# Optimization experiments

Hardware: AMD Instinct MI355X
Metric: run time of the kernel (lower is better)

## Reference

```python
import jax, jax.numpy as jnp
import numpy as np

B, T, D = 16, 4096, 256
CODEBOOK_SIZE = 1024
COMMITMENT = 1.0


def setup_inputs() -> dict:
    key = jax.random.key(0)
    kx, kc = jax.random.split(key)
    x = jax.random.normal(kx, (B, T, D), dtype=jnp.float32)
    codebook = jax.random.normal(kc, (CODEBOOK_SIZE, D), dtype=jnp.float32)
    return {"x": x, "codebook": codebook}


def reference(x, codebook):
    # x: [B, T, D] continuous latents; codebook: [K, D]
    flat = x.reshape(-1, x.shape[-1])  # [N, D]
    # does not affect argmin but is kept for faithfulness to torch.cdist-style math)
    x_sq = jnp.sum(flat * flat, axis=1, keepdims=True)            # [N, 1]
    c_sq = jnp.sum(codebook * codebook, axis=1)                   # [K]
    dist = x_sq - 2.0 * (flat @ codebook.T) + c_sq[None, :]       # [N, K]
    indices = jnp.argmin(dist, axis=1)                            # [N] int
    quantized = codebook[indices].reshape(x.shape)                # gather, [B, T, D]
    # commitment loss: encoder pulled toward (stopped) codes
    commit_loss = COMMITMENT * jnp.mean(
        (x - jax.lax.stop_gradient(quantized)) ** 2
    )
    # straight-through estimator
    out = x + jax.lax.stop_gradient(quantized - x)
    return out, indices.reshape(x.shape[:-1]), commit_loss
```

## Files before the change

### kernel.cpp

```cpp
#include <hip/hip_runtime.h>

#define N_TOK 65536
#define DIM   256
#define KCODE 1024

#define NTHREADS 256
#define TM 128
#define TN 128
#define BK 32
#define NCHUNK 8
#define NSTAGE 8
#define OTM 128

#define REFINE_EPS 0.125f
#define TIE_THETA 1.0e-4

#define WS_CSQ_OFF   16
#define WS_IDX_OFF   2048
#define WS_PAIRS_OFF (WS_IDX_OFF + N_TOK)
#define WS_CBPK_OFF  (WS_PAIRS_OFF + N_TOK * NCHUNK * 4)

typedef float f32x4  __attribute__((ext_vector_type(4)));
typedef short bf16x8 __attribute__((ext_vector_type(8)));
typedef short s16x8  __attribute__((ext_vector_type(8)));

__global__ void rowsq_np_kernel(const float* __restrict__ m,
                                float* __restrict__ out,
                                float* __restrict__ loss_ws, int rows) {
#pragma clang fp contract(off)
    if (blockIdx.x == 0 && threadIdx.x == 0) loss_ws[0] = 0.0f;
    int row = blockIdx.x * 16 + (threadIdx.x >> 4);
    int l   = threadIdx.x & 15;
    if (row >= rows) return;
    int h = l >> 3;
    int j = l & 7;
    const float* p = m + (size_t)row * DIM + h * 128 + j;
    float v = p[0];
    float r = v * v;
#pragma unroll
    for (int i = 1; i < 16; ++i) {
        float w  = p[i * 8];
        float w2 = w * w;
        r = r + w2;
    }
    float t = r + __shfl_xor(r, 1);
    t = t + __shfl_xor(t, 2);
    t = t + __shfl_xor(t, 4);
    t = t + __shfl_xor(t, 8);
    if (l == 0) out[row] = t;
}

__device__ __forceinline__ void ins2(float d, int idx,
                                     float& d1, int& i1, float& d2, int& i2) {
    if (d < d1 || (d == d1 && idx < i1)) {
        d2 = d1; i2 = i1; d1 = d; i1 = idx;
    } else if ((d < d2 || (d == d2 && idx < i2)) && idx != i1) {
        d2 = d; i2 = idx;
    }
}

__device__ __forceinline__ void f2bf_split(float v, short& hi, short& lo) {
    unsigned u = __float_as_uint(v);
    unsigned r = (u + 0x7fffu + ((u >> 16) & 1u)) >> 16;
    hi = (short)r;
    float hf = __uint_as_float(r << 16);
    float lf = v - hf;
    unsigned u2 = __float_as_uint(lf);
    unsigned r2 = (u2 + 0x7fffu + ((u2 >> 16) & 1u)) >> 16;
    lo = (short)r2;
}

__global__ void pack_tiles_kernel(const float* __restrict__ src,
                                  unsigned short* __restrict__ dst,
                                  int total) {
    int tid = blockIdx.x * blockDim.x + threadIdx.x;
    if (tid >= total) return;
    int s   = tid & 3;
    int r   = (tid >> 2) & 127;
    int kc  = (tid >> 9) & 7;
    int g   = tid >> 12;
    int oct = s ^ ((r >> 1) & 3);

    const float4* xr = reinterpret_cast<const float4*>(
        src + ((size_t)(g * 128 + r)) * DIM + kc * 32 + oct * 8);
    float4 v0 = xr[0];
    float4 v1 = xr[1];

    float f[8] = {v0.x, v0.y, v0.z, v0.w, v1.x, v1.y, v1.z, v1.w};
    s16x8 hv, lv;
#pragma unroll
    for (int i = 0; i < 8; ++i) {
        short h, l;
        f2bf_split(f[i], h, l);
        hv[i] = h; lv[i] = l;
    }
    size_t base_hi = (((size_t)(g * 16 + kc) * 128 + r) << 5) + s * 8;
    size_t base_lo = (((size_t)(g * 16 + 8 + kc) * 128 + r) << 5) + s * 8;
    *reinterpret_cast<s16x8*>(dst + base_hi) = hv;
    *reinterpret_cast<s16x8*>(dst + base_lo) = lv;
}

__device__ __forceinline__ void gload_lds16(const unsigned short* g, unsigned short* lds) {
    __builtin_amdgcn_global_load_lds(
        (const __attribute__((address_space(1))) unsigned int*)g,
        (__attribute__((address_space(3))) unsigned int*)lds, 16, 0, 0);
}

__launch_bounds__(NTHREADS, 2)
__global__ void vq_main_kernel(const unsigned short* __restrict__ xpk,
                               const unsigned short* __restrict__ cbpk,
                               const float* __restrict__ csq,
                               float4* __restrict__ pairs) {
    __shared__ __align__(16) unsigned short shbuf[2][4 * 4096];
    __shared__ float4 pairs_sh[TM][2];

    const int tid  = threadIdx.x;
    const int w    = tid >> 6;
    const int wy   = w >> 1;
    const int wx   = w & 1;
    const int lane = tid & 63;
    const int lm   = lane & 15;
    const int q    = lane >> 4;

    const int bx     = blockIdx.x;
    const int jj     = bx >> 3;
    const int grp    = (bx & 7) + ((jj >> 3) << 3);
    const int cchunk = jj & 7;
    const int tok0   = grp * TM;
    const int code0  = cchunk * TN;

    float cs_reg[4];
#pragma unroll
    for (int ni = 0; ni < 4; ++ni)
        cs_reg[ni] = csq[code0 + wx * 64 + ni * 16 + lm];

    f32x4 acc[4][4];
#pragma unroll
    for (int mi = 0; mi < 4; ++mi)
#pragma unroll
        for (int ni = 0; ni < 4; ++ni)
            acc[mi][ni] = (f32x4){0.f, 0.f, 0.f, 0.f};

    int offA[4], offB[4];
#pragma unroll
    for (int mi = 0; mi < 4; ++mi) {
        int r = wy * 64 + mi * 16 + lm;
        offA[mi] = r * BK + ((q ^ ((r >> 1) & 3)) * 8);
    }
#pragma unroll
    for (int ni = 0; ni < 4; ++ni) {
        int r = wx * 64 + ni * 16 + lm;
        offB[ni] = r * BK + ((q ^ ((r >> 1) & 3)) * 8);
    }

    const int lsrc = w * 1024 + lane * 8;
    auto stage = [&](int p, int kc) {
        const unsigned short* gah = xpk  + (((size_t)(grp    * 16 +     kc)) << 12) + lsrc;
        const unsigned short* gal = xpk  + (((size_t)(grp    * 16 + 8 + kc)) << 12) + lsrc;
        const unsigned short* gbh = cbpk + (((size_t)(cchunk * 16 +     kc)) << 12) + lsrc;
        const unsigned short* gbl = cbpk + (((size_t)(cchunk * 16 + 8 + kc)) << 12) + lsrc;
        unsigned short* base = &shbuf[p][w * 1024];
        gload_lds16(gah,       base);
        gload_lds16(gah + 512, base + 512);
        gload_lds16(gal,       base + 4096);
        gload_lds16(gal + 512, base + 4096 + 512);
        gload_lds16(gbh,       base + 8192);
        gload_lds16(gbh + 512, base + 8192 + 512);
        gload_lds16(gbl,       base + 12288);
        gload_lds16(gbl + 512, base + 12288 + 512);
    };

    stage(0, 0);
    __syncthreads();

    int p = 0;
#pragma unroll 1
    for (int kc = 0; kc < NSTAGE; ++kc) {
        if (kc < NSTAGE - 1) stage(p ^ 1, kc + 1);

        const unsigned short* buf = &shbuf[p][0];
        bf16x8 ah[4], al[4], bh[4], bl[4];
#pragma unroll
        for (int mi = 0; mi < 4; ++mi) {
            ah[mi] = *reinterpret_cast<const bf16x8*>(buf + offA[mi]);
            al[mi] = *reinterpret_cast<const bf16x8*>(buf + 4096 + offA[mi]);
        }
#pragma unroll
        for (int ni = 0; ni < 4; ++ni) {
            bh[ni] = *reinterpret_cast<const bf16x8*>(buf + 8192 + offB[ni]);
            bl[ni] = *reinterpret_cast<const bf16x8*>(buf + 12288 + offB[ni]);
        }

        __builtin_amdgcn_s_setprio(1);
#pragma unroll
        for (int mi = 0; mi < 4; ++mi)
#pragma unroll
            for (int ni = 0; ni < 4; ++ni)
                acc[mi][ni] = __builtin_amdgcn_mfma_f32_16x16x32_bf16(
                    ah[mi], bh[ni], acc[mi][ni], 0, 0, 0);
#pragma unroll
        for (int mi = 0; mi < 4; ++mi)
#pragma unroll
            for (int ni = 0; ni < 4; ++ni)
                acc[mi][ni] = __builtin_amdgcn_mfma_f32_16x16x32_bf16(
                    ah[mi], bl[ni], acc[mi][ni], 0, 0, 0);
#pragma unroll
        for (int mi = 0; mi < 4; ++mi)
#pragma unroll
            for (int ni = 0; ni < 4; ++ni)
                acc[mi][ni] = __builtin_amdgcn_mfma_f32_16x16x32_bf16(
                    al[mi], bh[ni], acc[mi][ni], 0, 0, 0);
        __builtin_amdgcn_s_setprio(0);

        __syncthreads();
        p ^= 1;
    }

#pragma unroll
    for (int mi = 0; mi < 4; ++mi) {
#pragma unroll
        for (int r = 0; r < 4; ++r) {
            int row_local = wy * 64 + mi * 16 + q * 4 + r;
            float l1 = 3.4e38f, l2 = 3.4e38f;
            int   j1 = 0x7fffffff, j2 = 0x7fffffff;
#pragma unroll
            for (int ni = 0; ni < 4; ++ni) {
                float d = cs_reg[ni] - 2.0f * acc[mi][ni][r];
                ins2(d, code0 + wx * 64 + ni * 16 + lm, l1, j1, l2, j2);
            }
#pragma unroll
            for (int m = 1; m < 16; m <<= 1) {
                float o1 = __shfl_xor(l1, m);
                int   p1 = __shfl_xor(j1, m);
                float o2 = __shfl_xor(l2, m);
                int   p2 = __shfl_xor(j2, m);
                ins2(o1, p1, l1, j1, l2, j2);
                ins2(o2, p2, l1, j1, l2, j2);
            }
            if (lm == 0) {
                float4 pr;
                pr.x = l1; pr.y = l2;
                pr.z = __int_as_float(j1); pr.w = __int_as_float(j2);
                pairs_sh[row_local][wx] = pr;
            }
        }
    }
    __syncthreads();
    if (tid < TM) {
        float4 pa = pairs_sh[tid][0];
        float4 pb = pairs_sh[tid][1];
        float d1 = pa.x, d2 = pa.y;
        int   i1 = __float_as_int(pa.z), i2 = __float_as_int(pa.w);
        ins2(pb.x, __float_as_int(pb.z), d1, i1, d2, i2);
        ins2(pb.y, __float_as_int(pb.w), d1, i1, d2, i2);
        float4 pr;
        pr.x = d1; pr.y = d2;
        pr.z = __int_as_float(i1); pr.w = __int_as_float(i2);
        pairs[(size_t)cchunk * N_TOK + tok0 + tid] = pr;
    }
}

__launch_bounds__(256)
__global__ void merge_output_kernel(const float* __restrict__ x,
                                    const float* __restrict__ cb,
                                    const float4* __restrict__ pairs,
                                    float* __restrict__ out_q,
                                    float* __restrict__ out_idx,
                                    float* __restrict__ loss_ws) {
    __shared__ int   sh_idx[OTM];
    __shared__ float wsum[4];
    const int tid  = threadIdx.x;
    const int tok0 = blockIdx.x * OTM;

    if (tid < OTM) {
        const int t = tok0 + tid;
        float4 p0 = pairs[t];
        float d1 = p0.x, d2 = p0.y;
        int   i1 = __float_as_int(p0.z), i2 = __float_as_int(p0.w);
#pragma unroll
        for (int c = 1; c < NCHUNK; ++c) {
            float4 p = pairs[(size_t)c * N_TOK + t];
            ins2(p.x, __float_as_int(p.z), d1, i1, d2, i2);
            ins2(p.y, __float_as_int(p.w), d1, i1, d2, i2);
        }

        int pick = i1;
        if (d2 - d1 < REFINE_EPS) {
            const float* xr = x + (size_t)t * DIM;
            const float* c1 = cb + (size_t)i1 * DIM;
            const float* c2 = cb + (size_t)i2 * DIM;
            double sA = 0.0, dA = 0.0, sB = 0.0, dB = 0.0;
            for (int k = 0; k < DIM; ++k) {
                double xv = (double)xr[k];
                double a  = (double)c1[k];
                double b  = (double)c2[k];
                sA += a * a; dA += xv * a;
                sB += b * b; dB += xv * b;
            }
            double DA  = sA - 2.0 * dA;
            double DB  = sB - 2.0 * dB;
            double gap = DB - DA;
            if (gap > TIE_THETA)       pick = i1;
            else if (gap < -TIE_THETA) pick = i2;
            else                       pick = (i1 < i2) ? i1 : i2;
        }
        sh_idx[tid] = pick;
        out_idx[t]  = (float)pick;
    }
    __syncthreads();

    float lsum = 0.0f;
    for (int t = 0; t < OTM; ++t) {
        int code = sh_idx[t];
        float qv = cb[(size_t)code * DIM + tid];
        float xv = x[(size_t)(tok0 + t) * DIM + tid];
        out_q[(size_t)(tok0 + t) * DIM + tid] = xv + (qv - xv);
        float df = xv - qv;
        lsum = fmaf(df, df, lsum);
    }

#pragma unroll
    for (int off = 1; off < 64; off <<= 1) lsum += __shfl_xor(lsum, off);
    if ((tid & 63) == 0) wsum[tid >> 6] = lsum;
    __syncthreads();
    if (tid == 0) atomicAdd(loss_ws, (wsum[0] + wsum[1]) + (wsum[2] + wsum[3]));
}

__global__ void finalize_kernel(const float* ws, float* out_loss) {
    if (threadIdx.x == 0) out_loss[0] = ws[0] * (1.0f / 16777216.0f);
}

extern "C" void kernel_launch(void* const* d_in, const int* in_sizes, int n_in,
                              void* d_out, int out_size, void* d_ws, size_t ws_size,
                              hipStream_t stream) {
    const float* x  = (const float*)d_in[0];
    const float* cb = (const float*)d_in[1];

    float* out      = (float*)d_out;
    float* out_q    = out;
    float* out_idx  = out + (size_t)N_TOK * DIM;
    float* out_loss = out_idx + N_TOK;

    float*  ws    = (float*)d_ws;
    float*  csq   = ws + WS_CSQ_OFF;
    float4* pairs = (float4*)(ws + WS_PAIRS_OFF);
    unsigned short* cbpk = (unsigned short*)(ws + WS_CBPK_OFF);
    unsigned short* xpk  = (unsigned short*)out_q;

    rowsq_np_kernel<<<KCODE / 16, 256, 0, stream>>>(cb, csq, ws, KCODE);
    pack_tiles_kernel<<<(N_TOK * 32) / 256, 256, 0, stream>>>(x, xpk, N_TOK * 32);
    pack_tiles_kernel<<<(KCODE * 32) / 256, 256, 0, stream>>>(cb, cbpk, KCODE * 32);
    vq_main_kernel<<<(N_TOK / TM) * NCHUNK, NTHREADS, 0, stream>>>(xpk, cbpk, csq, pairs);
    merge_output_kernel<<<N_TOK / OTM, 256, 0, stream>>>(x, cb, pairs, out_q, out_idx, ws);
    finalize_kernel<<<1, 64, 0, stream>>>(ws, out_loss);
}
```

Baseline: 889.1 us.

## Stream codebook operands from global/L2 and stage only token tiles in LDS

The main GEMM kernel no longer stages codebook tiles in LDS. Each wave reads its codebook fragments directly from global memory, which is expected to hit L2 because the codebook is small. Only token tiles are double-buffered in shared memory, with the codebook pack left unswizzled to match. The three bf16 split-precision products (hi*hi, hi*lo, lo*hi) are serialized into 24 stages of 16 MFMAs each, which shrinks LDS and register footprint so launch bounds can target 4 blocks per CU. The trade-off is more barriers per block and global-load latency on the B operand inside the loop.

```diff
diff --git a/kernel.cpp b/kernel.cpp
--- a/kernel.cpp
+++ b/kernel.cpp
@@ -9,7 +9,7 @@
 #define TN 128
 #define BK 32
 #define NCHUNK 8
-#define NSTAGE 8
+#define NSTAGE 24
 #define OTM 128
 
 #define REFINE_EPS 0.125f
@@ -72,14 +72,14 @@
 
 __global__ void pack_tiles_kernel(const float* __restrict__ src,
                                   unsigned short* __restrict__ dst,
-                                  int total) {
+                                  int total, int swz) {
     int tid = blockIdx.x * blockDim.x + threadIdx.x;
     if (tid >= total) return;
     int s   = tid & 3;
     int r   = (tid >> 2) & 127;
     int kc  = (tid >> 9) & 7;
     int g   = tid >> 12;
-    int oct = s ^ ((r >> 1) & 3);
+    int oct = swz ? (s ^ ((r >> 1) & 3)) : s;
 
     const float4* xr = reinterpret_cast<const float4*>(
         src + ((size_t)(g * 128 + r)) * DIM + kc * 32 + oct * 8);
@@ -106,12 +106,12 @@
         (__attribute__((address_space(3))) unsigned int*)lds, 16, 0, 0);
 }
 
-__launch_bounds__(NTHREADS, 2)
+__launch_bounds__(NTHREADS, 4)
 __global__ void vq_main_kernel(const unsigned short* __restrict__ xpk,
                                const unsigned short* __restrict__ cbpk,
                                const float* __restrict__ csq,
                                float4* __restrict__ pairs) {
-    __shared__ __align__(16) unsigned short shbuf[2][4 * 4096];
+    __shared__ __align__(16) unsigned short shbuf[2][TM * BK];
     __shared__ float4 pairs_sh[TM][2];
 
     const int tid  = threadIdx.x;
@@ -141,33 +141,27 @@
         for (int ni = 0; ni < 4; ++ni)
             acc[mi][ni] = (f32x4){0.f, 0.f, 0.f, 0.f};
 
-    int offA[4], offB[4];
+    int offA[4];
 #pragma unroll
     for (int mi = 0; mi < 4; ++mi) {
         int r = wy * 64 + mi * 16 + lm;
         offA[mi] = r * BK + ((q ^ ((r >> 1) & 3)) * 8);
     }
+    int offB[4];
 #pragma unroll
     for (int ni = 0; ni < 4; ++ni) {
         int r = wx * 64 + ni * 16 + lm;
-        offB[ni] = r * BK + ((q ^ ((r >> 1) & 3)) * 8);
+        offB[ni] = r * BK + q * 8;
     }
 
     const int lsrc = w * 1024 + lane * 8;
-    auto stage = [&](int p, int kc) {
-        const unsigned short* gah = xpk  + (((size_t)(grp    * 16 +     kc)) << 12) + lsrc;
-        const unsigned short* gal = xpk  + (((size_t)(grp    * 16 + 8 + kc)) << 12) + lsrc;
-        const unsigned short* gbh = cbpk + (((size_t)(cchunk * 16 +     kc)) << 12) + lsrc;
-        const unsigned short* gbl = cbpk + (((size_t)(cchunk * 16 + 8 + kc)) << 12) + lsrc;
-        unsigned short* base = &shbuf[p][w * 1024];
-        gload_lds16(gah,       base);
-        gload_lds16(gah + 512, base + 512);
-        gload_lds16(gal,       base + 4096);
-        gload_lds16(gal + 512, base + 4096 + 512);
-        gload_lds16(gbh,       base + 8192);
-        gload_lds16(gbh + 512, base + 8192 + 512);
-        gload_lds16(gbl,       base + 12288);
-        gload_lds16(gbl + 512, base + 12288 + 512);
+    auto stage = [&](int p, int s) {
+        const int kc = s & 7;
+        const int pa = (s >= 16) ? 8 : 0;
+        const unsigned short* ga = xpk + (((size_t)(grp * 16 + pa + kc)) << 12) + lsrc;
+        unsigned short* At = &shbuf[p][w * 1024];
+        gload_lds16(ga,       At);
+        gload_lds16(ga + 512, At + 512);
     };
 
     stage(0, 0);
@@ -175,21 +169,23 @@
 
     int p = 0;
 #pragma unroll 1
-    for (int kc = 0; kc < NSTAGE; ++kc) {
-        if (kc < NSTAGE - 1) stage(p ^ 1, kc + 1);
+    for (int s = 0; s < NSTAGE; ++s) {
+        const int kc = s & 7;
+        const int pb = (s >= 8 && s < 16) ? 8 : 0;
+        const unsigned short* gb =
+            cbpk + (((size_t)(cchunk * 16 + pb + kc)) << 12);
+        bf16x8 bf[4];
+#pragma unroll
+        for (int ni = 0; ni < 4; ++ni)
+            bf[ni] = *reinterpret_cast<const bf16x8*>(gb + offB[ni]);
+
+        if (s < NSTAGE - 1) stage(p ^ 1, s + 1);
 
         const unsigned short* buf = &shbuf[p][0];
-        bf16x8 ah[4], al[4], bh[4], bl[4];
-#pragma unroll
-        for (int mi = 0; mi < 4; ++mi) {
-            ah[mi] = *reinterpret_cast<const bf16x8*>(buf + offA[mi]);
-            al[mi] = *reinterpret_cast<const bf16x8*>(buf + 4096 + offA[mi]);
-        }
-#pragma unroll
-        for (int ni = 0; ni < 4; ++ni) {
-            bh[ni] = *reinterpret_cast<const bf16x8*>(buf + 8192 + offB[ni]);
-            bl[ni] = *reinterpret_cast<const bf16x8*>(buf + 12288 + offB[ni]);
-        }
+        bf16x8 af[4];
+#pragma unroll
+        for (int mi = 0; mi < 4; ++mi)
+            af[mi] = *reinterpret_cast<const bf16x8*>(buf + offA[mi]);
 
         __builtin_amdgcn_s_setprio(1);
 #pragma unroll
@@ -197,19 +193,7 @@
 #pragma unroll
             for (int ni = 0; ni < 4; ++ni)
                 acc[mi][ni] = __builtin_amdgcn_mfma_f32_16x16x32_bf16(
-                    ah[mi], bh[ni], acc[mi][ni], 0, 0, 0);
-#pragma unroll
-        for (int mi = 0; mi < 4; ++mi)
-#pragma unroll
-            for (int ni = 0; ni < 4; ++ni)
-                acc[mi][ni] = __builtin_amdgcn_mfma_f32_16x16x32_bf16(
-                    ah[mi], bl[ni], acc[mi][ni], 0, 0, 0);
-#pragma unroll
-        for (int mi = 0; mi < 4; ++mi)
-#pragma unroll
-            for (int ni = 0; ni < 4; ++ni)
-                acc[mi][ni] = __builtin_amdgcn_mfma_f32_16x16x32_bf16(
-                    al[mi], bh[ni], acc[mi][ni], 0, 0, 0);
+                    af[mi], bf[ni], acc[mi][ni], 0, 0, 0);
         __builtin_amdgcn_s_setprio(0);
 
         __syncthreads();
@@ -348,8 +332,8 @@
     unsigned short* xpk  = (unsigned short*)out_q;
 
     rowsq_np_kernel<<<KCODE / 16, 256, 0, stream>>>(cb, csq, ws, KCODE);
-    pack_tiles_kernel<<<(N_TOK * 32) / 256, 256, 0, stream>>>(x, xpk, N_TOK * 32);
-    pack_tiles_kernel<<<(KCODE * 32) / 256, 256, 0, stream>>>(cb, cbpk, KCODE * 32);
+    pack_tiles_kernel<<<(N_TOK * 32) / 256, 256, 0, stream>>>(x, xpk, N_TOK * 32, 1);
+    pack_tiles_kernel<<<(KCODE * 32) / 256, 256, 0, stream>>>(cb, cbpk, KCODE * 32, 0);
     vq_main_kernel<<<(N_TOK / TM) * NCHUNK, NTHREADS, 0, stream>>>(xpk, cbpk, csq, pairs);
     merge_output_kernel<<<N_TOK / OTM, 256, 0, stream>>>(x, cb, pairs, out_q, out_idx, ws);
     finalize_kernel<<<1, 64, 0, stream>>>(ws, out_loss);
```

Measured after the change: 793.9 us. 10.7% less time.
